# Kernel optimization log

Hardware: AMD Instinct MI355X
Metric: run time of the kernel (lower is better)

The kernel has to match this reference:

```python
import jax, jax.numpy as jnp
import numpy as np

B, S, D, H = 8, 1024, 1024, 16
DK = D // H
NEG = -1e9


def setup_inputs() -> dict:
    key = jax.random.key(0)
    ks = jax.random.split(key, 11)
    s = 1.0 / np.sqrt(D)
    inp = {
        "query": jax.random.normal(ks[0], (B, S, D), jnp.float32),
        "key": jax.random.normal(ks[1], (B, S, D), jnp.float32),
        "value": jax.random.normal(ks[2], (B, S, D), jnp.float32),
        "mask": jnp.tril(jnp.ones((S, S), jnp.int32))[None, None],  # causal [1,1,S,S]
        "w_q": jax.random.normal(ks[3], (D, D), jnp.float32) * s,
        "b_q": jnp.zeros((D,), jnp.float32),
        "w_k": jax.random.normal(ks[4], (D, D), jnp.float32) * s,
        "b_k": jnp.zeros((D,), jnp.float32),
        "w_v": jax.random.normal(ks[5], (D, D), jnp.float32) * s,
        "b_v": jnp.zeros((D,), jnp.float32),
        "w_o": jax.random.normal(ks[6], (D, D), jnp.float32) * s,
        "b_o": jnp.zeros((D,), jnp.float32),
    }
    return inp


def reference(query, key, value, mask, w_q, b_q, w_k, b_k, w_v, b_v, w_o, b_o):
    # projections; weights stored as [in, out] (torch Linear applies x @ W.T; here
    # we use x @ W which is the same math with W = torch_W.T)
    def proj(x, w, b):
        # [B,S,D] -> [B,H,S,DK]
        y = x @ w + b
        return y.reshape(B, S, H, DK).transpose(0, 2, 1, 3)

    q = proj(query, w_q, b_q)
    k = proj(key, w_k, b_k)
    v = proj(value, w_v, b_v)

    scores = jnp.einsum("bhqd,bhkd->bhqk", q, k) / jnp.sqrt(jnp.float32(DK))
    scores = jnp.where(mask == 0, jnp.float32(NEG), scores)
    probs = jax.nn.softmax(scores, axis=-1)
    # dropout: eval mode (identity) for deterministic reference
    ctx = jnp.einsum("bhqk,bhkd->bhqd", probs, v)
    ctx = ctx.transpose(0, 2, 1, 3).reshape(B, S, D)
    return ctx @ w_o + b_o
```

## Files before the change

### kernel.cpp

```cpp
#include <hip/hip_runtime.h>

#define B_ 8
#define S_ 1024
#define D_ 1024
#define H_ 16
#define DK_ 64
#define M_ (B_ * S_)
#define NEGINF -1e38f

typedef __bf16 bf16_t;
typedef __bf16 bf16x8 __attribute__((ext_vector_type(8)));
typedef float f32x4 __attribute__((ext_vector_type(4)));
typedef unsigned int u32;

__device__ inline f32x4 mfma_bf16(bf16x8 a, bf16x8 b, f32x4 c) {
    return __builtin_amdgcn_mfma_f32_16x16x32_bf16(a, b, c, 0, 0, 0);
}

typedef const __attribute__((address_space(1))) u32* gas1_t;
typedef __attribute__((address_space(3))) u32* las3_t;
__device__ inline void gl_lds16(const void* g, void* l) {
    __builtin_amdgcn_global_load_lds((gas1_t)g, (las3_t)l, 16, 0, 0);
}

__device__ inline bf16x8 load8(const bf16_t* p) { return *(const bf16x8*)p; }
__device__ inline bf16x8 load8(const float* p) {
    const f32x4 a = *(const f32x4*)p;
    const f32x4 b = *(const f32x4*)(p + 4);
    bf16x8 r;
    r[0] = (bf16_t)a[0]; r[1] = (bf16_t)a[1];
    r[2] = (bf16_t)a[2]; r[3] = (bf16_t)a[3];
    r[4] = (bf16_t)b[0]; r[5] = (bf16_t)b[1];
    r[6] = (bf16_t)b[2]; r[7] = (bf16_t)b[3];
    return r;
}
__device__ inline void store_elem(bf16_t* Y, size_t i, float v) { Y[i] = (bf16_t)v; }
__device__ inline void store_elem(float* Y, size_t i, float v) { Y[i] = v; }

__global__ __launch_bounds__(256) void transpose4(
    const float* __restrict__ i0, const float* __restrict__ i1,
    const float* __restrict__ i2, const float* __restrict__ i3,
    bf16_t* __restrict__ o0, bf16_t* __restrict__ o1,
    bf16_t* __restrict__ o2, bf16_t* __restrict__ o3) {
    const float* ins[4] = {i0, i1, i2, i3};
    bf16_t* outs[4] = {o0, o1, o2, o3};
    const float* in = ins[blockIdx.z];
    bf16_t* out = outs[blockIdx.z];
    __shared__ __align__(16) bf16_t t[32][33];
    const int n0 = blockIdx.x * 32, k0 = blockIdx.y * 32;
    const int tx = threadIdx.x;
    for (int i = threadIdx.y; i < 32; i += 8)
        t[i][tx] = (bf16_t)in[(size_t)(k0 + i) * D_ + n0 + tx];
    __syncthreads();
    for (int i = threadIdx.y; i < 32; i += 8)
        out[(size_t)(n0 + i) * D_ + k0 + tx] = t[tx][i];
}

template <int MODE, typename TX, typename TY>
__global__ __launch_bounds__(256) void gemm_bt(
    const TX* __restrict__ X, const bf16_t* __restrict__ Wt,
    const float* __restrict__ bias, TY* __restrict__ Y, float scale) {
    __shared__ __align__(16) bf16_t As[128 * 32];
    __shared__ __align__(16) bf16_t Bs[128 * 32];
    const int tid = threadIdx.x;
    const int lane = tid & 63, wave = tid >> 6;
    const int ln = lane & 15, quad = lane >> 4;
    const int wm = (wave & 1) * 64, wn = (wave >> 1) * 64;
    const int m0 = blockIdx.x * 128, n0 = blockIdx.y * 128;

    const int srow = tid >> 2, scc = (tid & 3) * 8;
    const TX* pa0 = X + (size_t)(m0 + srow) * D_ + scc;
    const TX* pa1 = pa0 + (size_t)64 * D_;
    const bf16_t* pb0 = Wt + (size_t)(n0 + srow) * D_ + scc;
    const bf16_t* pb1 = pb0 + (size_t)64 * D_;
    bf16_t* qa0 = As + srow * 32 + scc;
    bf16_t* qa1 = As + (srow + 64) * 32 + scc;

    f32x4 acc[4][4] = {};
    for (int k0 = 0; k0 < D_; k0 += 32) {
        if constexpr (sizeof(TX) == 2) {
            gl_lds16(pa0 + k0, As + wave * 512);
            gl_lds16(pa1 + k0, As + 2048 + wave * 512);
        } else {
            *(bf16x8*)qa0 = load8(pa0 + k0);
            *(bf16x8*)qa1 = load8(pa1 + k0);
        }
        gl_lds16(pb0 + k0, Bs + wave * 512);
        gl_lds16(pb1 + k0, Bs + 2048 + wave * 512);
        __syncthreads();
        bf16x8 af[4], bfr[4];
#pragma unroll
        for (int mt = 0; mt < 4; mt++)
            af[mt] = *(const bf16x8*)(As + (wm + mt * 16 + ln) * 32 + quad * 8);
#pragma unroll
        for (int nt = 0; nt < 4; nt++)
            bfr[nt] = *(const bf16x8*)(Bs + (wn + nt * 16 + ln) * 32 + quad * 8);
#pragma unroll
        for (int mt = 0; mt < 4; mt++)
#pragma unroll
            for (int nt = 0; nt < 4; nt++)
                acc[mt][nt] = mfma_bf16(af[mt], bfr[nt], acc[mt][nt]);
        __syncthreads();
    }

#pragma unroll
    for (int mt = 0; mt < 4; mt++) {
#pragma unroll
        for (int nt = 0; nt < 4; nt++) {
#pragma unroll
            for (int r = 0; r < 4; r++) {
                const int m = m0 + wm + mt * 16 + quad * 4 + r;
                const int n = n0 + wn + nt * 16 + ln;
                const float v = (acc[mt][nt][r] + bias[n]) * scale;
                size_t idx;
                if (MODE == 0) {
                    idx = (size_t)m * D_ + n;
                } else {
                    const int b = m >> 10, s = m & 1023;
                    const int h = n >> 6, d = n & 63;
                    if (MODE == 1)
                        idx = ((size_t)(b * H_ + h) * S_ + s) * DK_ + d;
                    else
                        idx = ((size_t)(b * H_ + h) * DK_ + d) * S_ + s;
                }
                store_elem(Y, idx, v);
            }
        }
    }
}

__global__ __launch_bounds__(256, 2) void MaskedMultiHeadAttention_90709709291709_kernel(
    const bf16_t* __restrict__ Q, const bf16_t* __restrict__ K,
    const bf16_t* __restrict__ Vt, bf16_t* __restrict__ ctx) {
    __shared__ __align__(16) bf16_t Ks[64 * 64];
    __shared__ __align__(16) bf16_t Vs[64 * 64];
    __shared__ __align__(16) bf16_t pbuf[4][32 * 64];

    const int bh = blockIdx.y;
    const int bx = blockIdx.x;
    const int tid = threadIdx.x;
    const int lane = tid & 63, wave = tid >> 6;
    const int ln = lane & 15, quad = lane >> 4;

    const bf16_t* Qb = Q + (size_t)bh * S_ * DK_;
    const bf16_t* Kb = K + (size_t)bh * S_ * DK_;
    const bf16_t* Vb = Vt + (size_t)bh * DK_ * S_;
    const int b = bh >> 4, h = bh & 15;

    bf16x8 ones8;
#pragma unroll
    for (int i = 0; i < 8; i++) ones8[i] = (bf16_t)1.0f;

    for (int pass = 0; pass < 2; pass++) {
        const int j = pass ? (7 - bx) : bx;
        const int qb = j * 128;
        const int wq = qb + wave * 32;

        bf16x8 qf[2][2];
#pragma unroll
        for (int mi = 0; mi < 2; mi++)
#pragma unroll
            for (int kk = 0; kk < 2; kk++)
                qf[mi][kk] = *(const bf16x8*)(
                    Qb + (size_t)(wq + mi * 16 + ln) * DK_ + kk * 32 + quad * 8);

        f32x4 o[2][4] = {};
        f32x4 ol[2] = {};

        const int kend = qb + 128;
        for (int kt = 0; kt < kend; kt += 64) {
#pragma unroll
            for (int c = tid; c < 512; c += 256) {
                const int row = c >> 3, ch = c & 7;
                const int pch = ch ^ (row & 7);
                *(f32x4*)(Ks + row * 64 + pch * 8) =
                    *(const f32x4*)(Kb + (size_t)(kt + row) * DK_ + ch * 8);
                *(f32x4*)(Vs + row * 64 + pch * 8) =
                    *(const f32x4*)(Vb + (size_t)row * S_ + kt + ch * 8);
            }
            __syncthreads();

            const bool act0 = kt <= wq + 15;
            const bool act1 = kt <= wq + 31;
            if (act1) {
                bf16_t* pb = pbuf[wave];
#pragma unroll
                for (int mi = 0; mi < 2; mi++) {
                    if (!(mi ? act1 : act0)) continue;
                    f32x4 s[4];
#pragma unroll
                    for (int nt = 0; nt < 4; nt++) {
                        f32x4 a = {};
#pragma unroll
                        for (int kk = 0; kk < 2; kk++) {
                            const bf16x8 kf = *(const bf16x8*)(
                                Ks + (nt * 16 + ln) * 64 +
                                (((kk * 4 + quad) ^ (ln & 7)) * 8));
                            a = mfma_bf16(qf[mi][kk], kf, a);
                        }
                        s[nt] = a;
                    }
                    const bool needmask = (kt + 63) > (wq + mi * 16);
#pragma unroll
                    for (int r = 0; r < 4; r++) {
                        const int row = wq + mi * 16 + quad * 4 + r;
                        const int prow = mi * 16 + quad * 4 + r;
#pragma unroll
                        for (int nt = 0; nt < 4; nt++) {
                            float v = s[nt][r];
                            if (needmask && (kt + nt * 16 + ln > row)) v = NEGINF;
                            const float p = __builtin_amdgcn_exp2f(v - 16.f);
                            const int col = nt * 16 + ln;
                            pb[prow * 64 + (((col >> 3) ^ (prow & 7)) * 8) +
                               (col & 7)] = (bf16_t)p;
                        }
                    }
                }
#pragma unroll
                for (int mi = 0; mi < 2; mi++) {
                    if (!(mi ? act1 : act0)) continue;
                    bf16x8 pf[2];
#pragma unroll
                    for (int kk = 0; kk < 2; kk++)
                        pf[kk] = *(const bf16x8*)(
                            pb + (mi * 16 + ln) * 64 +
                            (((kk * 4 + quad) ^ (ln & 7)) * 8));
#pragma unroll
                    for (int kk = 0; kk < 2; kk++)
                        ol[mi] = mfma_bf16(pf[kk], ones8, ol[mi]);
#pragma unroll
                    for (int dk = 0; dk < 4; dk++)
#pragma unroll
                        for (int kk = 0; kk < 2; kk++) {
                            const bf16x8 vf = *(const bf16x8*)(
                                Vs + (dk * 16 + ln) * 64 +
                                (((kk * 4 + quad) ^ (ln & 7)) * 8));
                            o[mi][dk] = mfma_bf16(pf[kk], vf, o[mi][dk]);
                        }
                }
            }
            __syncthreads();
        }

#pragma unroll
        for (int mi = 0; mi < 2; mi++)
#pragma unroll
            for (int r = 0; r < 4; r++) {
                const float inv = 1.f / ol[mi][r];
                const int row = wq + mi * 16 + quad * 4 + r;
                const size_t base = ((size_t)b * S_ + row) * D_ + h * DK_;
#pragma unroll
                for (int dk = 0; dk < 4; dk++)
                    ctx[base + dk * 16 + ln] = (bf16_t)(o[mi][dk][r] * inv);
            }
    }
}

__global__ __launch_bounds__(256) void copy16(const f32x4* __restrict__ src,
                                              f32x4* __restrict__ dst, int n4) {
    const int i = blockIdx.x * 256 + threadIdx.x;
    if (i < n4) dst[i] = src[i];
}

extern "C" void kernel_launch(void* const* d_in, const int* in_sizes, int n_in,
                              void* d_out, int out_size, void* d_ws,
                              size_t ws_size, hipStream_t stream) {
    const float* query = (const float*)d_in[0];
    const float* key = (const float*)d_in[1];
    const float* value = (const float*)d_in[2];
    const float* w_q = (const float*)d_in[4];
    const float* b_q = (const float*)d_in[5];
    const float* w_k = (const float*)d_in[6];
    const float* b_k = (const float*)d_in[7];
    const float* w_v = (const float*)d_in[8];
    const float* b_v = (const float*)d_in[9];
    const float* w_o = (const float*)d_in[10];
    const float* b_o = (const float*)d_in[11];

    bf16_t* ws = (bf16_t*)d_ws;
    const size_t M8 = (size_t)M_ * D_;
    bf16_t* Qw = ws;
    bf16_t* Kw = ws + M8;
    bf16_t* Vw = ws + 2 * M8;
    bf16_t* wtq = ws + 3 * M8;
    bf16_t* wtk = wtq + (size_t)D_ * D_;
    bf16_t* wtv = wtk + (size_t)D_ * D_;
    bf16_t* wto = wtv + (size_t)D_ * D_;
    bf16_t* Cw = (bf16_t*)d_out;
    float* Yw = (float*)ws;

    transpose4<<<dim3(32, 32, 4), dim3(32, 8, 1), 0, stream>>>(
        w_q, w_k, w_v, w_o, wtq, wtk, wtv, wto);

    const dim3 gg(M_ / 128, D_ / 128, 1);
    const float qscale = 0.125f * 1.4426950408889634f;
    gemm_bt<1><<<gg, 256, 0, stream>>>(query, wtq, b_q, Qw, qscale);
    gemm_bt<1><<<gg, 256, 0, stream>>>(key, wtk, b_k, Kw, 1.0f);
    gemm_bt<2><<<gg, 256, 0, stream>>>(value, wtv, b_v, Vw, 1.0f);

    MaskedMultiHeadAttention_90709709291709_kernel<<<dim3(4, B_ * H_, 1), 256,
                                                     0, stream>>>(Qw, Kw, Vw,
                                                                  Cw);

    gemm_bt<0><<<gg, 256, 0, stream>>>(Cw, wto, b_o, Yw, 1.0f);
    const int n4 = (int)((M8 * 4) / 16);
    copy16<<<dim3((n4 + 255) / 256), 256, 0, stream>>>((const f32x4*)Yw,
                                                       (f32x4*)d_out, n4);
}
```

Baseline: 362.6 us.

## Pre-convert inputs to bf16, use async LDS loads with k-major tile layout

Adds a standalone fp32-to-bf16 conversion kernel so every projection GEMM can stage A tiles with direct global-to-LDS loads. The LDS tile layout changes to k-chunk-major (quad*1024 + row*8), with each wave loading one 8-wide k slice for 64 rows. When the workspace is large enough, the attention output goes to the workspace, so the output GEMM writes straight to d_out and the extra copy kernel is skipped. The trade is three extra conversion passes over the inputs and more kernel launches.

```diff
diff --git a/kernel.cpp b/kernel.cpp
--- a/kernel.cpp
+++ b/kernel.cpp
@@ -23,8 +23,7 @@
     __builtin_amdgcn_global_load_lds((gas1_t)g, (las3_t)l, 16, 0, 0);
 }
 
-__device__ inline bf16x8 load8(const bf16_t* p) { return *(const bf16x8*)p; }
-__device__ inline bf16x8 load8(const float* p) {
+__device__ inline bf16x8 load8f(const float* p) {
     const f32x4 a = *(const f32x4*)p;
     const f32x4 b = *(const f32x4*)(p + 4);
     bf16x8 r;
@@ -36,6 +35,12 @@
 }
 __device__ inline void store_elem(bf16_t* Y, size_t i, float v) { Y[i] = (bf16_t)v; }
 __device__ inline void store_elem(float* Y, size_t i, float v) { Y[i] = v; }
+
+__global__ __launch_bounds__(256) void f2b(const float* __restrict__ x,
+                                           bf16_t* __restrict__ y, int n8) {
+    const int i = blockIdx.x * 256 + threadIdx.x;
+    if (i < n8) *(bf16x8*)(y + (size_t)i * 8) = load8f(x + (size_t)i * 8);
+}
 
 __global__ __launch_bounds__(256) void transpose4(
     const float* __restrict__ i0, const float* __restrict__ i1,
@@ -56,45 +61,44 @@
         out[(size_t)(n0 + i) * D_ + k0 + tx] = t[tx][i];
 }
 
-template <int MODE, typename TX, typename TY>
+template <int MODE, typename TY>
 __global__ __launch_bounds__(256) void gemm_bt(
-    const TX* __restrict__ X, const bf16_t* __restrict__ Wt,
+    const bf16_t* __restrict__ X, const bf16_t* __restrict__ Wt,
     const float* __restrict__ bias, TY* __restrict__ Y, float scale) {
-    __shared__ __align__(16) bf16_t As[128 * 32];
-    __shared__ __align__(16) bf16_t Bs[128 * 32];
+    __shared__ __align__(16) bf16_t As[4096];
+    __shared__ __align__(16) bf16_t Bs[4096];
     const int tid = threadIdx.x;
     const int lane = tid & 63, wave = tid >> 6;
     const int ln = lane & 15, quad = lane >> 4;
     const int wm = (wave & 1) * 64, wn = (wave >> 1) * 64;
     const int m0 = blockIdx.x * 128, n0 = blockIdx.y * 128;
 
-    const int srow = tid >> 2, scc = (tid & 3) * 8;
-    const TX* pa0 = X + (size_t)(m0 + srow) * D_ + scc;
-    const TX* pa1 = pa0 + (size_t)64 * D_;
-    const bf16_t* pb0 = Wt + (size_t)(n0 + srow) * D_ + scc;
-    const bf16_t* pb1 = pb0 + (size_t)64 * D_;
-    bf16_t* qa0 = As + srow * 32 + scc;
-    bf16_t* qa1 = As + (srow + 64) * 32 + scc;
+    const bf16_t* pa[2];
+    const bf16_t* pb[2];
+    bf16_t *qa[2], *qb[2];
+#pragma unroll
+    for (int j = 0; j < 2; j++) {
+        pa[j] = X + (size_t)(m0 + j * 64 + lane) * D_ + wave * 8;
+        pb[j] = Wt + (size_t)(n0 + j * 64 + lane) * D_ + wave * 8;
+        qa[j] = As + wave * 1024 + j * 512;
+        qb[j] = Bs + wave * 1024 + j * 512;
+    }
 
     f32x4 acc[4][4] = {};
     for (int k0 = 0; k0 < D_; k0 += 32) {
-        if constexpr (sizeof(TX) == 2) {
-            gl_lds16(pa0 + k0, As + wave * 512);
-            gl_lds16(pa1 + k0, As + 2048 + wave * 512);
-        } else {
-            *(bf16x8*)qa0 = load8(pa0 + k0);
-            *(bf16x8*)qa1 = load8(pa1 + k0);
+#pragma unroll
+        for (int j = 0; j < 2; j++) {
+            gl_lds16(pa[j] + k0, qa[j]);
+            gl_lds16(pb[j] + k0, qb[j]);
         }
-        gl_lds16(pb0 + k0, Bs + wave * 512);
-        gl_lds16(pb1 + k0, Bs + 2048 + wave * 512);
         __syncthreads();
         bf16x8 af[4], bfr[4];
 #pragma unroll
         for (int mt = 0; mt < 4; mt++)
-            af[mt] = *(const bf16x8*)(As + (wm + mt * 16 + ln) * 32 + quad * 8);
+            af[mt] = *(const bf16x8*)(As + quad * 1024 + (wm + mt * 16 + ln) * 8);
 #pragma unroll
         for (int nt = 0; nt < 4; nt++)
-            bfr[nt] = *(const bf16x8*)(Bs + (wn + nt * 16 + ln) * 32 + quad * 8);
+            bfr[nt] = *(const bf16x8*)(Bs + quad * 1024 + (wn + nt * 16 + ln) * 8);
 #pragma unroll
         for (int mt = 0; mt < 4; mt++)
 #pragma unroll
@@ -286,24 +290,37 @@
     bf16_t* wtk = wtq + (size_t)D_ * D_;
     bf16_t* wtv = wtk + (size_t)D_ * D_;
     bf16_t* wto = wtv + (size_t)D_ * D_;
-    bf16_t* Cw = (bf16_t*)d_out;
-    float* Yw = (float*)ws;
+    bf16_t* Xb = (bf16_t*)d_out + M8;
+
+    const bool bigws = ws_size >= (size_t)36 * M8 / 8 * 2;
+    bf16_t* Cw = bigws ? (ws + (size_t)28 * 1024 * 1024) : (bf16_t*)d_out;
 
     transpose4<<<dim3(32, 32, 4), dim3(32, 8, 1), 0, stream>>>(
         w_q, w_k, w_v, w_o, wtq, wtk, wtv, wto);
 
     const dim3 gg(M_ / 128, D_ / 128, 1);
+    const int n8 = (int)(M8 / 8);
+    const dim3 cg((n8 + 255) / 256);
     const float qscale = 0.125f * 1.4426950408889634f;
-    gemm_bt<1><<<gg, 256, 0, stream>>>(query, wtq, b_q, Qw, qscale);
-    gemm_bt<1><<<gg, 256, 0, stream>>>(key, wtk, b_k, Kw, 1.0f);
-    gemm_bt<2><<<gg, 256, 0, stream>>>(value, wtv, b_v, Vw, 1.0f);
+
+    f2b<<<cg, 256, 0, stream>>>(query, Xb, n8);
+    gemm_bt<1><<<gg, 256, 0, stream>>>(Xb, wtq, b_q, Qw, qscale);
+    f2b<<<cg, 256, 0, stream>>>(key, Xb, n8);
+    gemm_bt<1><<<gg, 256, 0, stream>>>(Xb, wtk, b_k, Kw, 1.0f);
+    f2b<<<cg, 256, 0, stream>>>(value, Xb, n8);
+    gemm_bt<2><<<gg, 256, 0, stream>>>(Xb, wtv, b_v, Vw, 1.0f);
 
     MaskedMultiHeadAttention_90709709291709_kernel<<<dim3(4, B_ * H_, 1), 256,
                                                      0, stream>>>(Qw, Kw, Vw,
                                                                   Cw);
 
-    gemm_bt<0><<<gg, 256, 0, stream>>>(Cw, wto, b_o, Yw, 1.0f);
-    const int n4 = (int)((M8 * 4) / 16);
-    copy16<<<dim3((n4 + 255) / 256), 256, 0, stream>>>((const f32x4*)Yw,
-                                                       (f32x4*)d_out, n4);
-}
+    if (bigws) {
+        gemm_bt<0><<<gg, 256, 0, stream>>>(Cw, wto, b_o, (float*)d_out, 1.0f);
+    } else {
+        float* Yw = (float*)ws;
+        gemm_bt<0><<<gg, 256, 0, stream>>>(Cw, wto, b_o, Yw, 1.0f);
+        const int n4 = (int)((M8 * 4) / 16);
+        copy16<<<dim3((n4 + 255) / 256), 256, 0, stream>>>((const f32x4*)Yw,
+                                                           (f32x4*)d_out, n4);
+    }
+}
```

Result: no change. 368.9 us (+1.8%).
